# Performance work log

Hardware: AMD Instinct MI355X
Metric: run time of the kernel (lower is better)

Reference implementation:

```python
import jax, jax.numpy as jnp
import numpy as np

N, E, F_IN, H, C = 10000, 640000, 128, 128, 40


def setup_inputs() -> dict:
    key = jax.random.key(0)
    ks = jax.random.split(key, 8)
    x = jax.random.normal(ks[0], (N, F_IN), dtype=jnp.float32)
    edge_index = jax.random.randint(ks[1], (2, E), 0, N, dtype=jnp.int64)
    W1 = jax.random.normal(ks[2], (F_IN, H), dtype=jnp.float32) / np.sqrt(F_IN)
    b1 = jnp.zeros((H,), dtype=jnp.float32)
    W2 = jax.random.normal(ks[3], (H, H), dtype=jnp.float32) / np.sqrt(H)
    b2 = jnp.zeros((H,), dtype=jnp.float32)
    Wc = jax.random.normal(ks[4], (H, C), dtype=jnp.float32) / np.sqrt(H)
    bc = jnp.zeros((C,), dtype=jnp.float32)
    return {"x": x, "edge_index": edge_index, "W1": W1, "b1": b1,
            "W2": W2, "b2": b2, "Wc": Wc, "bc": bc}


def _gcn_conv(x, src, dst, norm, W, b):
    # GCNConv: out = D^{-1/2}(A+I)D^{-1/2} (x @ W) + b
    h = x @ W                               # [N, H]
    msg = h[src] * norm[:, None]            # gather + per-edge normalize
    out = jax.ops.segment_sum(msg, dst, num_segments=N)  # scatter-add
    return out + b


def reference(x, edge_index, W1, b1, W2, b2, Wc, bc):
    # add self-loops (as PyG GCNConv does by default)
    loops = jnp.arange(N, dtype=edge_index.dtype)
    src = jnp.concatenate([edge_index[0], loops])   # [E+N]
    dst = jnp.concatenate([edge_index[1], loops])   # [E+N]
    # symmetric normalization deg^{-1/2} with self-loops included
    deg = jax.ops.segment_sum(jnp.ones_like(dst, dtype=x.dtype), dst, num_segments=N)
    dinv = jax.lax.rsqrt(deg)                       # deg >= 1 due to self-loops
    norm = dinv[src] * dinv[dst]                    # [E+N]

    h = _gcn_conv(x, src, dst, norm, W1, b1)
    h = jax.nn.relu(h)
    h = _gcn_conv(h, src, dst, norm, W2, b2)
    logits = h @ Wc + bc                            # [N, C]
    return jax.nn.log_softmax(logits, axis=1)
```

## Files before the change

kernel.cpp:

```cpp
#include <hip/hip_runtime.h>
#include <hip/hip_fp16.h>
#include <math.h>

#define FDIM 128
#define CDIM 40
#define DMAX 192
#define NMAX 10240
#define SLICE_SHIFT 14
#define SLICE_SZ (1 << SLICE_SHIFT)

__device__ __forceinline__ uint2 pack_half4(float4 v) {
    __half2 p0 = __float22half2_rn(make_float2(v.x, v.y));
    __half2 p1 = __float22half2_rn(make_float2(v.z, v.w));
    uint2 u;
    u.x = *(unsigned int*)&p0;
    u.y = *(unsigned int*)&p1;
    return u;
}

__device__ __forceinline__ void unpack_add4(float acc[8], uint4 r) {
    __half2* p = (__half2*)&r;
    #pragma unroll
    for (int q = 0; q < 4; ++q) {
        float2 f = __half22float2(p[q]);
        acc[2 * q]     += f.x;
        acc[2 * q + 1] += f.y;
    }
}

__global__ __launch_bounds__(256) void k_hist(
        const int* __restrict__ dst, unsigned short* __restrict__ lrank,
        int* __restrict__ cnt, int e, int n) {
    __shared__ int h[NMAX];
    int tid = threadIdx.x;
    for (int i = tid; i < n; i += 256) h[i] = 0;
    __syncthreads();
    int base = (int)blockIdx.x << SLICE_SHIFT;
    int end = base + SLICE_SZ; if (end > e) end = e;
    for (int i = base + tid * 4; i < end; i += 1024) {
        if (i + 3 < end) {
            int4 d = *(const int4*)(dst + i);
            int p0 = atomicAdd(&h[d.x], 1);
            int p1 = atomicAdd(&h[d.y], 1);
            int p2 = atomicAdd(&h[d.z], 1);
            int p3 = atomicAdd(&h[d.w], 1);
            ushort4 r;
            r.x = (unsigned short)p0; r.y = (unsigned short)p1;
            r.z = (unsigned short)p2; r.w = (unsigned short)p3;
            *(ushort4*)(lrank + i) = r;
        } else {
            for (int k = i; k < end; ++k)
                lrank[k] = (unsigned short)atomicAdd(&h[dst[k]], 1);
        }
    }
    __syncthreads();
    int* c = cnt + (size_t)blockIdx.x * n;
    for (int i = tid; i < n; i += 256) c[i] = h[i];
}

__global__ __launch_bounds__(256) void k_scan(
        int* __restrict__ cnt, int* __restrict__ deg, int nslice, int n) {
    int v = blockIdx.x * 256 + threadIdx.x;
    if (v >= n) return;
    int s = 0;
    for (int b = 0; b < nslice; ++b) {
        int t = cnt[(size_t)b * n + v];
        cnt[(size_t)b * n + v] = s;
        s += t;
    }
    deg[v] = s;
}

__global__ __launch_bounds__(256) void k_mega(
        const float* __restrict__ A, const float* __restrict__ W,
        const int* __restrict__ deg, uint2* __restrict__ h16, int n,
        const int* __restrict__ src, const int* __restrict__ dst,
        const unsigned short* __restrict__ lrank, const int* __restrict__ base,
        unsigned short* __restrict__ col, int e, int gemm_blocks) {
    __shared__ float As[32][FDIM];
    int tid = threadIdx.x;
    if ((int)blockIdx.x < gemm_blocks) {
        int r0 = blockIdx.x * 32;
        for (int t = tid; t < 32 * 32; t += 256) {
            int r = t >> 5, c4 = t & 31;
            int gr = r0 + r;
            float4 v = make_float4(0.f, 0.f, 0.f, 0.f);
            if (gr < n) v = ((const float4*)A)[(size_t)gr * 32 + c4];
            ((float4*)As[r])[c4] = v;
        }
        __syncthreads();
        int cb = (tid & 31) * 4;
        int rb = (tid >> 5) * 4;
        float4 acc0 = make_float4(0,0,0,0), acc1 = acc0, acc2 = acc0, acc3 = acc0;
        for (int k = 0; k < FDIM; ++k) {
            float4 w = *(const float4*)(W + k * FDIM + cb);
            float a0 = As[rb + 0][k], a1 = As[rb + 1][k];
            float a2 = As[rb + 2][k], a3 = As[rb + 3][k];
            acc0.x += a0 * w.x; acc0.y += a0 * w.y; acc0.z += a0 * w.z; acc0.w += a0 * w.w;
            acc1.x += a1 * w.x; acc1.y += a1 * w.y; acc1.z += a1 * w.z; acc1.w += a1 * w.w;
            acc2.x += a2 * w.x; acc2.y += a2 * w.y; acc2.z += a2 * w.z; acc2.w += a2 * w.w;
            acc3.x += a3 * w.x; acc3.y += a3 * w.y; acc3.z += a3 * w.z; acc3.w += a3 * w.w;
        }
        float4 accs[4] = {acc0, acc1, acc2, acc3};
        #pragma unroll
        for (int i = 0; i < 4; ++i) {
            int gr = r0 + rb + i;
            if (gr < n) {
                float dinv = rsqrtf((float)(deg[gr] + 1));
                float4 v = accs[i];
                v.x *= dinv; v.y *= dinv; v.z *= dinv; v.w *= dinv;
                h16[(size_t)gr * 32 + (cb >> 2)] = pack_half4(v);
            }
        }
    } else {
        int g = ((int)blockIdx.x - gemm_blocks) * 256 + tid;
        int i4 = g * 4;
        if (i4 + 3 < e) {
            const int* bs = base + (size_t)(i4 >> SLICE_SHIFT) * n;
            int4 d = ((const int4*)dst)[g];
            int4 s = ((const int4*)src)[g];
            ushort4 lr = ((const ushort4*)lrank)[g];
            int p0 = bs[d.x] + lr.x;
            int p1 = bs[d.y] + lr.y;
            int p2 = bs[d.z] + lr.z;
            int p3 = bs[d.w] + lr.w;
            if (p0 < DMAX) col[(size_t)d.x * DMAX + p0] = (unsigned short)s.x;
            if (p1 < DMAX) col[(size_t)d.y * DMAX + p1] = (unsigned short)s.y;
            if (p2 < DMAX) col[(size_t)d.z * DMAX + p2] = (unsigned short)s.z;
            if (p3 < DMAX) col[(size_t)d.w * DMAX + p3] = (unsigned short)s.w;
        } else if (i4 < e) {
            for (int k = i4; k < e; ++k) {
                int d = dst[k];
                int p = base[(size_t)(k >> SLICE_SHIFT) * n + d] + lrank[k];
                if (p < DMAX) col[(size_t)d * DMAX + p] = (unsigned short)src[k];
            }
        }
    }
}

template <bool RELU>
__device__ __forceinline__ void agg_gather(
        float out8[8], const uint4* __restrict__ hs,
        const unsigned short* __restrict__ col, const int* __restrict__ deg,
        const float* __restrict__ bias, int node, int l) {
    int dn = deg[node];
    float dinv = rsqrtf((float)(dn + 1));
    if (dn > DMAX) dn = DMAX;
    const uint4* cl8 = (const uint4*)(col + (size_t)node * DMAX);
    float a0[8], a1[8];
    #pragma unroll
    for (int q = 0; q < 8; ++q) { a0[q] = 0.f; a1[q] = 0.f; }
    unpack_add4(a0, hs[(size_t)node * 16 + l]);
    int j = 0;
    for (; j + 8 <= dn; j += 8) {
        uint4 c = cl8[j >> 3];
        int s0 = c.x & 0xFFFF, s1 = c.x >> 16;
        int s2 = c.y & 0xFFFF, s3 = c.y >> 16;
        int s4 = c.z & 0xFFFF, s5 = c.z >> 16;
        int s6 = c.w & 0xFFFF, s7 = c.w >> 16;
        uint4 q0 = hs[(size_t)s0 * 16 + l];
        uint4 q1 = hs[(size_t)s1 * 16 + l];
        uint4 q2 = hs[(size_t)s2 * 16 + l];
        uint4 q3 = hs[(size_t)s3 * 16 + l];
        uint4 q4 = hs[(size_t)s4 * 16 + l];
        uint4 q5 = hs[(size_t)s5 * 16 + l];
        uint4 q6 = hs[(size_t)s6 * 16 + l];
        uint4 q7 = hs[(size_t)s7 * 16 + l];
        unpack_add4(a0, q0); unpack_add4(a1, q1);
        unpack_add4(a0, q2); unpack_add4(a1, q3);
        unpack_add4(a0, q4); unpack_add4(a1, q5);
        unpack_add4(a0, q6); unpack_add4(a1, q7);
    }
    const unsigned short* cl = col + (size_t)node * DMAX;
    for (; j < dn; ++j) unpack_add4(a0, hs[(size_t)cl[j] * 16 + l]);
    float4 b0 = ((const float4*)bias)[2 * l];
    float4 b1 = ((const float4*)bias)[2 * l + 1];
    float bb[8] = {b0.x, b0.y, b0.z, b0.w, b1.x, b1.y, b1.z, b1.w};
    #pragma unroll
    for (int q = 0; q < 8; ++q) {
        float v = dinv * (a0[q] + a1[q]) + bb[q];
        out8[q] = RELU ? fmaxf(v, 0.f) : v;
    }
}

__global__ __launch_bounds__(128) void k_agg_gemm(
        const uint4* __restrict__ hs1, const unsigned short* __restrict__ col,
        const int* __restrict__ deg, const float* __restrict__ b1,
        const float* __restrict__ W2, uint2* __restrict__ hs2, int n) {
    __shared__ float As[8][FDIM + 4];
    __shared__ float dl[8];
    int tid = threadIdx.x;
    int grp = tid >> 4, l = tid & 15;
    int node = blockIdx.x * 8 + grp;
    if (node < n) {
        float r8[8];
        agg_gather<true>(r8, hs1, col, deg, b1, node, l);
        float4* dst4 = (float4*)&As[grp][8 * l];
        dst4[0] = make_float4(r8[0], r8[1], r8[2], r8[3]);
        dst4[1] = make_float4(r8[4], r8[5], r8[6], r8[7]);
        if (l == 0) dl[grp] = rsqrtf((float)(deg[node] + 1));
    }
    __syncthreads();
    int cb = (tid & 31) * 4;
    int rb = (tid >> 5) * 2;
    float4 acc0 = make_float4(0,0,0,0), acc1 = acc0;
    for (int k = 0; k < FDIM; ++k) {
        float4 w = *(const float4*)(W2 + k * FDIM + cb);
        float x0 = As[rb][k], x1 = As[rb + 1][k];
        acc0.x += x0 * w.x; acc0.y += x0 * w.y; acc0.z += x0 * w.z; acc0.w += x0 * w.w;
        acc1.x += x1 * w.x; acc1.y += x1 * w.y; acc1.z += x1 * w.z; acc1.w += x1 * w.w;
    }
    int g0 = blockIdx.x * 8 + rb;
    if (g0 < n) {
        float s = dl[rb];
        float4 v = acc0;
        v.x *= s; v.y *= s; v.z *= s; v.w *= s;
        hs2[(size_t)g0 * 32 + (cb >> 2)] = pack_half4(v);
    }
    if (g0 + 1 < n) {
        float s = dl[rb + 1];
        float4 v = acc1;
        v.x *= s; v.y *= s; v.z *= s; v.w *= s;
        hs2[(size_t)(g0 + 1) * 32 + (cb >> 2)] = pack_half4(v);
    }
}

__global__ __launch_bounds__(128) void k_agg_cls(
        const uint4* __restrict__ hs2, const unsigned short* __restrict__ col,
        const int* __restrict__ deg, const float* __restrict__ b2,
        const float* __restrict__ Wc, const float* __restrict__ bc,
        float* __restrict__ out, int n) {
    __shared__ float As[8][FDIM + 4];
    int tid = threadIdx.x;
    int grp = tid >> 4, l = tid & 15;
    int node = blockIdx.x * 8 + grp;
    if (node < n) {
        float r8[8];
        agg_gather<false>(r8, hs2, col, deg, b2, node, l);
        float4* dst4 = (float4*)&As[grp][8 * l];
        dst4[0] = make_float4(r8[0], r8[1], r8[2], r8[3]);
        dst4[1] = make_float4(r8[4], r8[5], r8[6], r8[7]);
    }
    __syncthreads();
    int wv = tid >> 6, lane = tid & 63;
    #pragma unroll
    for (int ii = 0; ii < 4; ++ii) {
        int li = wv * 4 + ii;
        int nd = blockIdx.x * 8 + li;
        if (nd >= n) continue;
        const float* row = As[li];
        int c = (lane < CDIM) ? lane : (lane - 24);
        float acc = bc[c];
        for (int k = 0; k < FDIM; k += 4) {
            float a0 = row[k + 0], a1 = row[k + 1];
            float a2 = row[k + 2], a3 = row[k + 3];
            acc += a0 * Wc[(k + 0) * CDIM + c];
            acc += a1 * Wc[(k + 1) * CDIM + c];
            acc += a2 * Wc[(k + 2) * CDIM + c];
            acc += a3 * Wc[(k + 3) * CDIM + c];
        }
        float lv = (lane < CDIM) ? acc : -INFINITY;
        float m = lv;
        for (int off = 32; off > 0; off >>= 1) m = fmaxf(m, __shfl_down(m, off));
        m = __shfl(m, 0);
        float e = (lane < CDIM) ? expf(lv - m) : 0.0f;
        float s = e;
        for (int off = 32; off > 0; off >>= 1) s += __shfl_down(s, off);
        s = __shfl(s, 0);
        if (lane < CDIM) out[(size_t)nd * CDIM + lane] = lv - m - logf(s);
    }
}


extern "C" void kernel_launch(void* const* d_in, const int* in_sizes, int n_in,
                              void* d_out, int out_size, void* d_ws, size_t ws_size,
                              hipStream_t stream) {
    const float* x  = (const float*)d_in[0];
    const int*   ei = (const int*)d_in[1];
    const float* W1 = (const float*)d_in[2];
    const float* b1 = (const float*)d_in[3];
    const float* W2 = (const float*)d_in[4];
    const float* b2 = (const float*)d_in[5];
    const float* Wc = (const float*)d_in[6];
    const float* bc = (const float*)d_in[7];
    float* out = (float*)d_out;

    const int N = in_sizes[0] / FDIM;
    const int E = in_sizes[1] / 2;
    const int* srcp = ei;
    const int* dstp = ei + E;
    const int NSLICE = (E + SLICE_SZ - 1) >> SLICE_SHIFT;

    char* ws = (char*)d_ws;
    auto alloc = [&](size_t bytes) {
        char* p = ws;
        ws += (bytes + 255) & ~(size_t)255;
        return p;
    };
    int*            deg   = (int*)           alloc((size_t)N * 4);
    int*            cnt   = (int*)           alloc((size_t)NSLICE * N * 4);
    unsigned short* lrank = (unsigned short*)alloc((size_t)E * 2);
    unsigned short* col   = (unsigned short*)alloc((size_t)N * DMAX * 2);
    uint4*          h1h   = (uint4*)         alloc((size_t)N * 256);
    uint4*          h2h   = (uint4*)         alloc((size_t)N * 256);

    k_hist<<<NSLICE, 256, 0, stream>>>(dstp, lrank, cnt, E, N);

    k_scan<<<(N + 255) / 256, 256, 0, stream>>>(cnt, deg, NSLICE, N);

    int gb = (N + 31) / 32;
    int fb = (E / 4 + 255) / 256;
    k_mega<<<gb + fb, 256, 0, stream>>>(
        x, W1, deg, (uint2*)h1h, N, srcp, dstp, lrank, cnt, col, E, gb);

    k_agg_gemm<<<(N + 7) / 8, 128, 0, stream>>>(
        h1h, col, deg, b1, W2, (uint2*)h2h, N);

    k_agg_cls<<<(N + 7) / 8, 128, 0, stream>>>(
        h2h, col, deg, b2, Wc, bc, out, N);
}
```

Measured before the change: 160.2 us.

## Use nontemporal stores, unroll gather by 16, and halve histogram slice size

Replaces the plain global stores of half-precision features, CSR column entries and the final output with nontemporal stores, so written data does not evict cached gather sources. Adds a 16-neighbor unrolled loop in the aggregation gather to keep more independent loads in flight. Halves the edge slice size used for the rank histogram, which creates more slices and a larger per-slice base table. Nontemporal stores to data that is read back soon may lose cache hits, and the wider unroll raises register pressure.

```diff
diff --git a/kernel.cpp b/kernel.cpp
--- a/kernel.cpp
+++ b/kernel.cpp
@@ -6,7 +6,7 @@
 #define CDIM 40
 #define DMAX 192
 #define NMAX 10240
-#define SLICE_SHIFT 14
+#define SLICE_SHIFT 13
 #define SLICE_SZ (1 << SLICE_SHIFT)
 
 __device__ __forceinline__ uint2 pack_half4(float4 v) {
@@ -16,6 +16,10 @@
     u.x = *(unsigned int*)&p0;
     u.y = *(unsigned int*)&p1;
     return u;
+}
+
+__device__ __forceinline__ void nt_store_u2(uint2* p, uint2 v) {
+    __builtin_nontemporal_store(*(unsigned long long*)&v, (unsigned long long*)p);
 }
 
 __device__ __forceinline__ void unpack_add4(float acc[8], uint4 r) {
@@ -109,7 +113,7 @@
                 float dinv = rsqrtf((float)(deg[gr] + 1));
                 float4 v = accs[i];
                 v.x *= dinv; v.y *= dinv; v.z *= dinv; v.w *= dinv;
-                h16[(size_t)gr * 32 + (cb >> 2)] = pack_half4(v);
+                nt_store_u2(&h16[(size_t)gr * 32 + (cb >> 2)], pack_half4(v));
             }
         }
     } else {
@@ -124,15 +128,15 @@
             int p1 = bs[d.y] + lr.y;
             int p2 = bs[d.z] + lr.z;
             int p3 = bs[d.w] + lr.w;
-            if (p0 < DMAX) col[(size_t)d.x * DMAX + p0] = (unsigned short)s.x;
-            if (p1 < DMAX) col[(size_t)d.y * DMAX + p1] = (unsigned short)s.y;
-            if (p2 < DMAX) col[(size_t)d.z * DMAX + p2] = (unsigned short)s.z;
-            if (p3 < DMAX) col[(size_t)d.w * DMAX + p3] = (unsigned short)s.w;
+            if (p0 < DMAX) __builtin_nontemporal_store((unsigned short)s.x, col + (size_t)d.x * DMAX + p0);
+            if (p1 < DMAX) __builtin_nontemporal_store((unsigned short)s.y, col + (size_t)d.y * DMAX + p1);
+            if (p2 < DMAX) __builtin_nontemporal_store((unsigned short)s.z, col + (size_t)d.z * DMAX + p2);
+            if (p3 < DMAX) __builtin_nontemporal_store((unsigned short)s.w, col + (size_t)d.w * DMAX + p3);
         } else if (i4 < e) {
             for (int k = i4; k < e; ++k) {
                 int d = dst[k];
                 int p = base[(size_t)(k >> SLICE_SHIFT) * n + d] + lrank[k];
-                if (p < DMAX) col[(size_t)d * DMAX + p] = (unsigned short)src[k];
+                if (p < DMAX) __builtin_nontemporal_store((unsigned short)src[k], col + (size_t)d * DMAX + p);
             }
         }
     }
@@ -152,6 +156,42 @@
     for (int q = 0; q < 8; ++q) { a0[q] = 0.f; a1[q] = 0.f; }
     unpack_add4(a0, hs[(size_t)node * 16 + l]);
     int j = 0;
+    for (; j + 16 <= dn; j += 16) {
+        uint4 cA = cl8[(j >> 3) + 0];
+        uint4 cB = cl8[(j >> 3) + 1];
+        int s0 = cA.x & 0xFFFF, s1 = cA.x >> 16;
+        int s2 = cA.y & 0xFFFF, s3 = cA.y >> 16;
+        int s4 = cA.z & 0xFFFF, s5 = cA.z >> 16;
+        int s6 = cA.w & 0xFFFF, s7 = cA.w >> 16;
+        int s8 = cB.x & 0xFFFF, s9 = cB.x >> 16;
+        int sa = cB.y & 0xFFFF, sb = cB.y >> 16;
+        int sc = cB.z & 0xFFFF, sd = cB.z >> 16;
+        int se = cB.w & 0xFFFF, sf = cB.w >> 16;
+        uint4 q0 = hs[(size_t)s0 * 16 + l];
+        uint4 q1 = hs[(size_t)s1 * 16 + l];
+        uint4 q2 = hs[(size_t)s2 * 16 + l];
+        uint4 q3 = hs[(size_t)s3 * 16 + l];
+        uint4 q4 = hs[(size_t)s4 * 16 + l];
+        uint4 q5 = hs[(size_t)s5 * 16 + l];
+        uint4 q6 = hs[(size_t)s6 * 16 + l];
+        uint4 q7 = hs[(size_t)s7 * 16 + l];
+        uint4 q8 = hs[(size_t)s8 * 16 + l];
+        uint4 q9 = hs[(size_t)s9 * 16 + l];
+        uint4 qa = hs[(size_t)sa * 16 + l];
+        uint4 qb = hs[(size_t)sb * 16 + l];
+        uint4 qc = hs[(size_t)sc * 16 + l];
+        uint4 qd = hs[(size_t)sd * 16 + l];
+        uint4 qe = hs[(size_t)se * 16 + l];
+        uint4 qf = hs[(size_t)sf * 16 + l];
+        unpack_add4(a0, q0); unpack_add4(a1, q1);
+        unpack_add4(a0, q2); unpack_add4(a1, q3);
+        unpack_add4(a0, q4); unpack_add4(a1, q5);
+        unpack_add4(a0, q6); unpack_add4(a1, q7);
+        unpack_add4(a0, q8); unpack_add4(a1, q9);
+        unpack_add4(a0, qa); unpack_add4(a1, qb);
+        unpack_add4(a0, qc); unpack_add4(a1, qd);
+        unpack_add4(a0, qe); unpack_add4(a1, qf);
+    }
     for (; j + 8 <= dn; j += 8) {
         uint4 c = cl8[j >> 3];
         int s0 = c.x & 0xFFFF, s1 = c.x >> 16;
@@ -215,13 +255,13 @@
         float s = dl[rb];
         float4 v = acc0;
         v.x *= s; v.y *= s; v.z *= s; v.w *= s;
-        hs2[(size_t)g0 * 32 + (cb >> 2)] = pack_half4(v);
+        nt_store_u2(&hs2[(size_t)g0 * 32 + (cb >> 2)], pack_half4(v));
     }
     if (g0 + 1 < n) {
         float s = dl[rb + 1];
         float4 v = acc1;
         v.x *= s; v.y *= s; v.z *= s; v.w *= s;
-        hs2[(size_t)(g0 + 1) * 32 + (cb >> 2)] = pack_half4(v);
+        nt_store_u2(&hs2[(size_t)(g0 + 1) * 32 + (cb >> 2)], pack_half4(v));
     }
 }
 
@@ -267,7 +307,8 @@
         float s = e;
         for (int off = 32; off > 0; off >>= 1) s += __shfl_down(s, off);
         s = __shfl(s, 0);
-        if (lane < CDIM) out[(size_t)nd * CDIM + lane] = lv - m - logf(s);
+        if (lane < CDIM)
+            __builtin_nontemporal_store(lv - m - logf(s), out + (size_t)nd * CDIM + lane);
     }
 }
 
```

Measured after the change: 184.9 us. 1.15x slower.
